# Optimization experiments

Measured on AMD Instinct MI355X. Metric: run time of the kernel, lower is better.

The kernel has to match this reference:

```python
import jax, jax.numpy as jnp
import numpy as np

ACT_BITS = 8
Q_B = 2 ** (ACT_BITS - 1)          # 128
EPS = 1e-6                          # module epsilon
GN_EPS = 1e-5                       # torch GroupNorm default eps
SCALE = 0.01                        # fixed ternary weight scale (buffer)
STRIDE = 1
PADDING = 1


def setup_inputs() -> dict:
    key = jax.random.key(0)
    k1, k2 = jax.random.split(key)
    x = jax.random.normal(k1, (16, 256, 64, 64), dtype=jnp.float32)
    weight = jax.random.normal(k2, (256, 256, 3, 3), dtype=jnp.float32)
    bias = jnp.zeros((256,), dtype=jnp.float32)
    ln_weight = jnp.ones((256,), dtype=jnp.float32)
    ln_bias = jnp.zeros((256,), dtype=jnp.float32)
    return {"x": x, "weight": weight, "bias": bias,
            "ln_weight": ln_weight, "ln_bias": ln_bias}


def _group_norm_1group(x, gamma, beta):
    # GroupNorm(1, C): normalize over (C, H, W) per sample, per-channel affine.
    mean = jnp.mean(x, axis=(1, 2, 3), keepdims=True)
    var = jnp.var(x, axis=(1, 2, 3), keepdims=True)
    xn = (x - mean) * jax.lax.rsqrt(var + GN_EPS)
    return xn * gamma[None, :, None, None] + beta[None, :, None, None]


def reference(x, weight, bias, ln_weight, ln_bias):
    # 1) GroupNorm
    x_ln = _group_norm_1group(x, ln_weight, ln_bias)

    # 2) BitNet absmax activation quantization (global absmax)
    gamma = jnp.maximum(jnp.max(jnp.abs(x_ln)), EPS)
    x_scaled = x_ln * (Q_B / gamma)
    x_clipped = jnp.clip(x_scaled, -Q_B + EPS, Q_B - EPS)
    x_quant = jnp.round(x_clipped)

    # 3) Ternary weight quantization with fixed scale: {-SCALE, 0, +SCALE}
    delta = 0.7 * jnp.mean(jnp.abs(weight))  # TTQ threshold
    w_q = jnp.where(weight > delta, SCALE,
                    jnp.where(weight < -delta, -SCALE, 0.0)).astype(weight.dtype)

    # 4) Conv2d (NCHW, OIHW)
    y = jax.lax.conv_general_dilated(
        x_quant, w_q,
        window_strides=(STRIDE, STRIDE),
        padding=[(PADDING, PADDING), (PADDING, PADDING)],
        dimension_numbers=("NCHW", "OIHW", "NCHW"),
        feature_group_count=1,
    )

    # 5) Dequant + bias
    y = y * (gamma / Q_B) + bias[None, :, None, None]
    return y
```

## Files before the change

### kernel.cpp

```cpp
#include <hip/hip_runtime.h>
#include <hip/hip_bf16.h>

#define CHW   1048576
#define XQ_BYTES 17842176u
#define WQ_OFF   17842176u
#define GNP_OFF  18432000u
#define CMM_OFF  18448384u
#define MR_OFF   18481152u
#define SC_OFF   18481280u
#define WP_OFF   18481296u
#define DL_OFF   18481584u
#define EVC_OFF  18481588u
#define EVL_OFF  18481592u

typedef __attribute__((ext_vector_type(4)))  int i32x4;
typedef __attribute__((ext_vector_type(16))) int i32x16;

__device__ __forceinline__ void gload16(const void* g, void* l) {
    __builtin_amdgcn_global_load_lds(
        (const __attribute__((address_space(1))) unsigned int*)(unsigned long long)(g),
        (__attribute__((address_space(3))) unsigned int*)(unsigned int)(unsigned long long)(l),
        16, 0, 0);
}

__global__ void k_pass1(const float* __restrict__ x, double2* __restrict__ part,
                        float2* __restrict__ cmm) {
    int bid = blockIdx.x;
    int n = bid >> 6, c4 = bid & 63;
    int t = threadIdx.x, ch = t >> 6, lane = t & 63;
    int c = c4 * 4 + ch;
    const float4* p = (const float4*)(x + (size_t)n * CHW + (size_t)c * 4096);
    double s = 0.0, ss = 0.0;
    float mn = 1e30f, mx = -1e30f;
#pragma unroll
    for (int k = 0; k < 16; ++k) {
        float4 v = p[k * 64 + lane];
        mn = fminf(mn, fminf(fminf(v.x, v.y), fminf(v.z, v.w)));
        mx = fmaxf(mx, fmaxf(fmaxf(v.x, v.y), fmaxf(v.z, v.w)));
        double dx = v.x, dy = v.y, dz = v.z, dw = v.w;
        s  += dx + dy + dz + dw;
        ss += dx * dx + dy * dy + dz * dz + dw * dw;
    }
    for (int o = 32; o; o >>= 1) {
        s += __shfl_down(s, o); ss += __shfl_down(ss, o);
        mn = fminf(mn, __shfl_down(mn, o)); mx = fmaxf(mx, __shfl_down(mx, o));
    }
    __shared__ double sh0[4], sh1[4];
    if (lane == 0) {
        cmm[n * 256 + c] = make_float2(mn, mx);
        sh0[ch] = s; sh1[ch] = ss;
    }
    __syncthreads();
    if (t == 0)
        part[bid] = make_double2(sh0[0] + sh0[1] + sh0[2] + sh0[3],
                                 sh1[0] + sh1[1] + sh1[2] + sh1[3]);
}

__global__ void k_wsum(const float* __restrict__ w, double* __restrict__ wp) {
    int blk = blockIdx.x, t = threadIdx.x;
    const float4* p = (const float4*)(w + (size_t)blk * 16384);
    double s = 0.0;
#pragma unroll
    for (int j = 0; j < 16; ++j) {
        float4 v = p[j * 256 + t];
        s += fabs((double)v.x) + fabs((double)v.y) + fabs((double)v.z) + fabs((double)v.w);
    }
    for (int o = 32; o; o >>= 1) s += __shfl_down(s, o);
    __shared__ double sh[4];
    if ((t & 63) == 0) sh[t >> 6] = s;
    __syncthreads();
    if (t == 0) wp[blk] = sh[0] + sh[1] + sh[2] + sh[3];
}

__global__ void k_scalars(const double2* __restrict__ part, const float2* __restrict__ cmm,
                          const float* __restrict__ lnw, const float* __restrict__ lnb,
                          const double* __restrict__ wp,
                          float2* __restrict__ mr, float* __restrict__ sc,
                          float* __restrict__ dl, int* __restrict__ evcnt) {
    __shared__ float shm[16], shr[16];
    int t = threadIdx.x;
    {
        int n = t >> 4, i = t & 15;
        double s = 0.0, ss = 0.0;
#pragma unroll
        for (int k = 0; k < 4; ++k) {
            double2 v = part[n * 64 + i * 4 + k];
            s += v.x; ss += v.y;
        }
        for (int o = 8; o; o >>= 1) { s += __shfl_down(s, o); ss += __shfl_down(ss, o); }
        if (i == 0) {
            double mean = s * (1.0 / 1048576.0);
            double var  = ss * (1.0 / 1048576.0) - mean * mean;
            shm[n] = (float)mean; shr[n] = (float)(1.0 / sqrt(var + 1e-5));
        }
    }
    __syncthreads();
    if (t < 16) mr[t] = make_float2(shm[t], shr[t]);
    if (t == 0) evcnt[0] = 0;
    float m = 0.0f;
#pragma unroll
    for (int k = 0; k < 16; ++k) {
        int idx = t + k * 256;
        int n = idx >> 8, c = idx & 255;
        float2 v = cmm[idx];
        float scale = lnw[c] * shr[n];
        float shift = lnb[c] - shm[n] * scale;
        m = fmaxf(m, fmaxf(fabsf(v.x * scale + shift), fabsf(v.y * scale + shift)));
    }
    for (int o = 32; o; o >>= 1) m = fmaxf(m, __shfl_down(m, o));
    __shared__ float shg[4];
    if ((t & 63) == 0) shg[t >> 6] = m;
    __syncthreads();
    if (t == 0) {
        float gamma = fmaxf(fmaxf(fmaxf(shg[0], shg[1]), fmaxf(shg[2], shg[3])), 1e-6f);
        sc[0] = gamma;
        sc[1] = 128.0f / gamma;
        sc[2] = (gamma / 128.0f) * 0.01f;
    }
    if (t < 64) {
        double s = (t < 36) ? wp[t] : 0.0;
        for (int o = 32; o; o >>= 1) s += __shfl_down(s, o);
        if (t == 0) dl[0] = (float)(0.7 * (s / 589824.0));
    }
}

__global__ void k_wquant(const float* __restrict__ w, const float* __restrict__ dl,
                         signed char* __restrict__ wq) {
    __shared__ float sw[2304];
    int co = blockIdx.x, t = threadIdx.x;
    const float* wr = w + (size_t)co * 2304;
#pragma unroll
    for (int j = 0; j < 9; ++j) sw[j * 256 + t] = wr[j * 256 + t];
    __syncthreads();
    float d = dl[0];
#pragma unroll
    for (int tap = 0; tap < 9; ++tap) {
        float v = sw[t * 9 + tap];
        int s = (v > d) ? 1 : ((v < -d) ? -1 : 0);
        wq[tap * 65536 + co * 256 + t] = (signed char)s;
    }
}

__global__ void k_halo(unsigned char* __restrict__ xq) {
    int idx = blockIdx.x * 8 + (threadIdx.x >> 5);
    int n = idx / 260, p = idx - n * 260;
    int hh, ww;
    if (p < 66)       { hh = 0;        ww = p; }
    else if (p < 132) { hh = 65;       ww = p - 66; }
    else if (p < 196) { hh = p - 131;  ww = 0; }
    else              { hh = p - 195;  ww = 65; }
    *(uint2*)(xq + ((size_t)(n * 66 + hh) * 66 + ww) * 256 + (threadIdx.x & 31) * 8) =
        make_uint2(0, 0);
}

__global__ void k_quantx(const float* __restrict__ x, const float2* __restrict__ mr,
                         const float* __restrict__ sc, const float* __restrict__ lnw,
                         const float* __restrict__ lnb, unsigned char* __restrict__ xq,
                         int* __restrict__ evcnt, int* __restrict__ evlist) {
    int bid = blockIdx.x;
    int n = bid >> 6, hg = (bid >> 2) & 15, cg = bid & 3;
    int t = threadIdx.x;
    int w = t & 63, h = hg * 4 + (t >> 6);
    float2 m = mr[n];
    float s128 = sc[1];
    uint u[16];
    const float* xp = x + (((size_t)n * 256 + cg * 64) * 64 + h) * 64 + w;
#pragma unroll
    for (int ci = 0; ci < 64; ++ci) {
        int c = cg * 64 + ci;
        float g = lnw[c] * m.y;
        float be = lnb[c];
        float v = xp[(size_t)ci * 4096];
        float xs = ((v - m.x) * g + be) * s128;
        xs = fminf(fmaxf(xs, -(128.0f - 1e-6f)), 128.0f - 1e-6f);
        int q = (int)rintf(xs);
        if (q == 128) {
            int idx = atomicAdd(evcnt, 1);
            if (idx < 1024) evlist[idx] = (n << 20) | (h << 14) | (w << 8) | c;
            q = 127;
        }
        uint b = (uint)(q & 255);
        if ((ci & 3) == 0) u[ci >> 2] = b; else u[ci >> 2] |= b << ((ci & 3) * 8);
    }
    unsigned char* op = xq + ((size_t)(n * 66 + h + 1) * 66 + (w + 1)) * 256 + cg * 64;
    uint4* o4 = (uint4*)op;
#pragma unroll
    for (int s2 = 0; s2 < 4; ++s2)
        o4[s2] = make_uint4(u[s2 * 4], u[s2 * 4 + 1], u[s2 * 4 + 2], u[s2 * 4 + 3]);
}

__global__ void k_fix(const signed char* __restrict__ wq, const int* __restrict__ evcnt,
                      const int* __restrict__ evlist, const float* __restrict__ sc,
                      float* __restrict__ out) {
    int cnt = *evcnt; if (cnt > 1024) cnt = 1024;
    float qs = sc[2];
    int co = threadIdx.x;
    for (int e = blockIdx.x; e < cnt; e += gridDim.x) {
        int pk = evlist[e];
        int n = pk >> 20, h = (pk >> 14) & 63, w = (pk >> 8) & 63, ci = pk & 255;
#pragma unroll
        for (int ty = 0; ty < 3; ++ty)
#pragma unroll
            for (int tx = 0; tx < 3; ++tx) {
                int i = h + 1 - ty, j = w + 1 - tx;
                if (i < 0 || i > 63 || j < 0 || j > 63) continue;
                int sgn = wq[(ty * 3 + tx) * 65536 + co * 256 + ci];
                if (sgn)
                    atomicAdd(out + (((size_t)n * 256 + co) * 64 + i) * 64 + j,
                              qs * (float)sgn);
            }
    }
}

#define ABUFB 32768
#define LD16(off) (*(const i32x4*)&lds8[(off)])
#define MFMA_I8(A, B, C) __builtin_amdgcn_mfma_i32_32x32x32_i8(A, B, C, 0, 0, 0)

#define STAGE_A(AS) { \
    const int _so = (AS) * ABUFB + wv * 1024; \
    gload16(aSrc + stA,         lds8 + _so); \
    gload16(aSrc + stA + 33792, lds8 + _so + 8192); \
    if (aKc < 3) { aKc++; stA += 64; } \
    else { aKc = 0; if (aTx < 2) { aTx++; stA += 64; } else { aTx = 0; stA += 16192; } } }

#define STAGE_B(BS) { \
    const int _so = (BS) * ABUFB + 16384 + wv * 1024; \
    gload16(bSrc + stB,         lds8 + _so); \
    gload16(bSrc + stB + 32768, lds8 + _so + 8192); \
    if (bKc < 3) { bKc++; stB += 64; } else { bKc = 0; stB += 65344; } }

#define PHASE(RB, SB, DO, W) { \
    const int _ab = (RB) * ABUFB; \
    const int _bb = (RB) * ABUFB + 16384; \
    i32x4 a00 = LD16(_ab + rdA),        a01 = LD16((_ab + rdA) ^ 32); \
    i32x4 a10 = LD16(_ab + rdA + 2048), a11 = LD16((_ab + rdA + 2048) ^ 32); \
    i32x4 a20 = LD16(_ab + rdA + 4096), a21 = LD16((_ab + rdA + 4096) ^ 32); \
    i32x4 a30 = LD16(_ab + rdA + 6144), a31 = LD16((_ab + rdA + 6144) ^ 32); \
    i32x4 b00 = LD16(_bb + rdB),        b01 = LD16((_bb + rdB) ^ 32); \
    i32x4 b10 = LD16(_bb + rdB + 2048), b11 = LD16((_bb + rdB + 2048) ^ 32); \
    if (DO) { STAGE_A(SB) STAGE_B(SB) } \
    __builtin_amdgcn_sched_barrier(0); \
    __builtin_amdgcn_s_barrier(); \
    asm volatile("s_waitcnt lgkmcnt(0)" ::: "memory"); \
    __builtin_amdgcn_sched_barrier(0); \
    __builtin_amdgcn_s_setprio(1); \
    acc[0][0] = MFMA_I8(a00, b00, acc[0][0]); acc[0][1] = MFMA_I8(a00, b10, acc[0][1]); \
    acc[1][0] = MFMA_I8(a10, b00, acc[1][0]); acc[1][1] = MFMA_I8(a10, b10, acc[1][1]); \
    acc[2][0] = MFMA_I8(a20, b00, acc[2][0]); acc[2][1] = MFMA_I8(a20, b10, acc[2][1]); \
    acc[3][0] = MFMA_I8(a30, b00, acc[3][0]); acc[3][1] = MFMA_I8(a30, b10, acc[3][1]); \
    acc[0][0] = MFMA_I8(a01, b01, acc[0][0]); acc[0][1] = MFMA_I8(a01, b11, acc[0][1]); \
    acc[1][0] = MFMA_I8(a11, b01, acc[1][0]); acc[1][1] = MFMA_I8(a11, b11, acc[1][1]); \
    acc[2][0] = MFMA_I8(a21, b01, acc[2][0]); acc[2][1] = MFMA_I8(a21, b11, acc[2][1]); \
    acc[3][0] = MFMA_I8(a31, b01, acc[3][0]); acc[3][1] = MFMA_I8(a31, b11, acc[3][1]); \
    __builtin_amdgcn_s_setprio(0); \
    if ((W) == 8)      { asm volatile("s_waitcnt vmcnt(8)" ::: "memory"); } \
    else if ((W) == 4) { asm volatile("s_waitcnt vmcnt(4)" ::: "memory"); } \
    else if ((W) == 0) { asm volatile("s_waitcnt vmcnt(0)" ::: "memory"); } \
    if ((W) >= 0) { __builtin_amdgcn_s_barrier(); __builtin_amdgcn_sched_barrier(0); } \
}

__global__ __launch_bounds__(512, 2) void k_conv(const unsigned char* __restrict__ xq,
                                                 const signed char* __restrict__ wq,
                                                 const float* __restrict__ sc,
                                                 const float* __restrict__ bias,
                                                 float* __restrict__ out) {
    __shared__ __align__(128) unsigned char lds8[163840];
    int t = threadIdx.x, wv = t >> 6, l = t & 63;
    int wm = wv >> 2, wn = wv & 3;
    int l31 = l & 31, l5 = l >> 5;

    int bid = ((int)blockIdx.x & 7) * 32 + ((int)blockIdx.x >> 3);
    int n = bid >> 4, h2 = (bid & 15) << 2;

    int s_src = (l & 7) ^ (l >> 3);
    int sb2   = (s_src >> 2) & 1;
    int skc   = s_src & 3;
    int RA    = wv * 16 + ((l >> 3) << 1) + sb2;
    int hsub  = RA >> 6, wA = RA & 63;
    const unsigned char* aSrc = xq +
        ((size_t)(n * 66 + h2 + hsub) * 66 + wA) * 256 + skc * 16;
    int coB = ((wv * 8 + (l >> 3)) << 1) + sb2;
    const unsigned char* bSrc = (const unsigned char*)wq + (size_t)coB * 256 + skc * 16;

    int q3    = (l31 >> 1) & 7;
    int s0    = ((l31 & 1) << 2) | l5;
    int phys0 = s0 ^ q3;
    int rdA = (wm * 64 + (l31 >> 1)) * 128 + phys0 * 16;
    int rdB = (wn * 32 + (l31 >> 1)) * 128 + phys0 * 16;

    i32x16 acc[4][2] = {};

    int stA = 0, aKc = 0, aTx = 0;
    int stB = 0, bKc = 0;
    STAGE_A(0) STAGE_B(0)
    STAGE_A(1) STAGE_B(1)
    STAGE_A(2) STAGE_B(2)
    asm volatile("s_waitcnt vmcnt(8)" ::: "memory");
    __builtin_amdgcn_s_barrier();
    __builtin_amdgcn_sched_barrier(0);

#pragma unroll 1
    for (int it = 0; it < 6; ++it) {
        PHASE(0, 3, 1, 8)
        PHASE(1, 4, 1, 8)
        PHASE(2, 0, 1, 8)
        PHASE(3, 1, 1, 8)
        PHASE(4, 2, 1, 8)
    }
    PHASE(0, 3, 1, 8)
    PHASE(1, 4, 1, 8)
    PHASE(2, 0, 1, 8)
    PHASE(3, 0, 0, 4)
    PHASE(4, 0, 0, 0)
    PHASE(0, 0, 0, -1)

    float qs = sc[2];
    float bv0 = bias[wn * 64 + l31];
    float bv1 = bias[wn * 64 + 32 + l31];
    __builtin_amdgcn_s_barrier();
    float4* lf = (float4*)lds8;
#pragma unroll
    for (int rh = 0; rh < 2; ++rh) {
#pragma unroll
        for (int mh = 0; mh < 2; ++mh) {
            int m = rh * 2 + mh;
#pragma unroll
            for (int nf = 0; nf < 2; ++nf) {
                int co = wn * 64 + nf * 32 + l31;
                float bv = nf ? bv1 : bv0;
                int rowb = (wm * 256 + co) * 16;
#pragma unroll
                for (int rg = 0; rg < 4; ++rg) {
                    int slot = mh * 8 + rg * 2 + l5;
                    float4 v;
                    v.x = (float)acc[m][nf][rg * 4 + 0] * qs + bv;
                    v.y = (float)acc[m][nf][rg * 4 + 1] * qs + bv;
                    v.z = (float)acc[m][nf][rg * 4 + 2] * qs + bv;
                    v.w = (float)acc[m][nf][rg * 4 + 3] * qs + bv;
                    lf[rowb + (slot ^ (co & 7))] = v;
                }
            }
        }
        __syncthreads();
#pragma unroll
        for (int i = 0; i < 16; ++i) {
            int idx = t + i * 512;
            int lw = idx & 15, co = (idx >> 4) & 255, hs = idx >> 12;
            float4 v = lf[(hs * 256 + co) * 16 + (lw ^ (co & 7))];
            int h = h2 + hs * 2 + rh;
            *(float4*)(out + ((size_t)(n * 256 + co) * 64 + h) * 64 + lw * 4) = v;
        }
        if (rh == 0) __syncthreads();
    }
}

extern "C" void kernel_launch(void* const* d_in, const int* in_sizes, int n_in,
                              void* d_out, int out_size, void* d_ws, size_t ws_size,
                              hipStream_t stream) {
    (void)in_sizes; (void)n_in; (void)out_size; (void)ws_size;
    const float* x    = (const float*)d_in[0];
    const float* wgt  = (const float*)d_in[1];
    const float* bias = (const float*)d_in[2];
    const float* lnw  = (const float*)d_in[3];
    const float* lnb  = (const float*)d_in[4];
    float* out = (float*)d_out;
    char* ws = (char*)d_ws;

    unsigned char* xq  = (unsigned char*)ws;
    signed char*   wq  = (signed char*)(ws + WQ_OFF);
    double2* gnp = (double2*)(ws + GNP_OFF);
    float2*  cmm = (float2*)(ws + CMM_OFF);
    float2*  mr  = (float2*)(ws + MR_OFF);
    float*   sc  = (float*)(ws + SC_OFF);
    double*  wp  = (double*)(ws + WP_OFF);
    float*   dl  = (float*)(ws + DL_OFF);
    int*     evc = (int*)(ws + EVC_OFF);
    int*     evl = (int*)(ws + EVL_OFF);

    k_pass1  <<<1024, 256, 0, stream>>>(x, gnp, cmm);
    k_wsum   <<<36,   256, 0, stream>>>(wgt, wp);
    k_scalars<<<1,    256, 0, stream>>>(gnp, cmm, lnw, lnb, wp, mr, sc, dl, evc);
    k_wquant <<<256,  256, 0, stream>>>(wgt, dl, wq);
    k_halo   <<<520,  256, 0, stream>>>(xq);
    k_quantx <<<1024, 256, 0, stream>>>(x, mr, sc, lnw, lnb, xq, evc, evl);
    k_conv   <<<256,  512, 0, stream>>>(xq, wq, sc, bias, out);
    k_fix    <<<64,   256, 0, stream>>>(wq, evc, evl, sc, out);
}
```

Measured before the change: 102.2 us.

## Double-buffer LDS fragments in registers to overlap reads with MFMAs

Restructures the conv main loop so LDS fragment reads for the next buffer are issued before the MFMAs of the current buffer, using two register sets (E/O) in a ping-pong pattern. The barrier and vmcnt wait move to the start of each phase, and the per-phase lgkmcnt(0) wait before the MFMAs is removed. The goal is to hide LDS read latency behind matrix math. In exchange it needs about 24 more VGPRs, which may pressure occupancy under launch_bounds(512,2). The vmcnt wait changes from 8 to 4, which may add stalls on global loads.

```diff
diff --git a/kernel.cpp b/kernel.cpp
--- a/kernel.cpp
+++ b/kernel.cpp
@@ -229,34 +229,34 @@
     gload16(bSrc + stB + 32768, lds8 + _so + 8192); \
     if (bKc < 3) { bKc++; stB += 64; } else { bKc = 0; stB += 65344; } }
 
-#define PHASE(RB, SB, DO, W) { \
-    const int _ab = (RB) * ABUFB; \
-    const int _bb = (RB) * ABUFB + 16384; \
-    i32x4 a00 = LD16(_ab + rdA),        a01 = LD16((_ab + rdA) ^ 32); \
-    i32x4 a10 = LD16(_ab + rdA + 2048), a11 = LD16((_ab + rdA + 2048) ^ 32); \
-    i32x4 a20 = LD16(_ab + rdA + 4096), a21 = LD16((_ab + rdA + 4096) ^ 32); \
-    i32x4 a30 = LD16(_ab + rdA + 6144), a31 = LD16((_ab + rdA + 6144) ^ 32); \
-    i32x4 b00 = LD16(_bb + rdB),        b01 = LD16((_bb + rdB) ^ 32); \
-    i32x4 b10 = LD16(_bb + rdB + 2048), b11 = LD16((_bb + rdB + 2048) ^ 32); \
-    if (DO) { STAGE_A(SB) STAGE_B(SB) } \
-    __builtin_amdgcn_sched_barrier(0); \
-    __builtin_amdgcn_s_barrier(); \
-    asm volatile("s_waitcnt lgkmcnt(0)" ::: "memory"); \
-    __builtin_amdgcn_sched_barrier(0); \
-    __builtin_amdgcn_s_setprio(1); \
-    acc[0][0] = MFMA_I8(a00, b00, acc[0][0]); acc[0][1] = MFMA_I8(a00, b10, acc[0][1]); \
-    acc[1][0] = MFMA_I8(a10, b00, acc[1][0]); acc[1][1] = MFMA_I8(a10, b10, acc[1][1]); \
-    acc[2][0] = MFMA_I8(a20, b00, acc[2][0]); acc[2][1] = MFMA_I8(a20, b10, acc[2][1]); \
-    acc[3][0] = MFMA_I8(a30, b00, acc[3][0]); acc[3][1] = MFMA_I8(a30, b10, acc[3][1]); \
-    acc[0][0] = MFMA_I8(a01, b01, acc[0][0]); acc[0][1] = MFMA_I8(a01, b11, acc[0][1]); \
-    acc[1][0] = MFMA_I8(a11, b01, acc[1][0]); acc[1][1] = MFMA_I8(a11, b11, acc[1][1]); \
-    acc[2][0] = MFMA_I8(a21, b01, acc[2][0]); acc[2][1] = MFMA_I8(a21, b11, acc[2][1]); \
-    acc[3][0] = MFMA_I8(a31, b01, acc[3][0]); acc[3][1] = MFMA_I8(a31, b11, acc[3][1]); \
-    __builtin_amdgcn_s_setprio(0); \
-    if ((W) == 8)      { asm volatile("s_waitcnt vmcnt(8)" ::: "memory"); } \
-    else if ((W) == 4) { asm volatile("s_waitcnt vmcnt(4)" ::: "memory"); } \
+#define LOADF(S, RB) { \
+    const int _ab = (RB) * ABUFB; const int _bb = _ab + 16384; \
+    S##a00 = LD16(_ab + rdA);        S##a01 = LD16((_ab + rdA) ^ 32); \
+    S##a10 = LD16(_ab + rdA + 2048); S##a11 = LD16((_ab + rdA + 2048) ^ 32); \
+    S##a20 = LD16(_ab + rdA + 4096); S##a21 = LD16((_ab + rdA + 4096) ^ 32); \
+    S##a30 = LD16(_ab + rdA + 6144); S##a31 = LD16((_ab + rdA + 6144) ^ 32); \
+    S##b00 = LD16(_bb + rdB);        S##b01 = LD16((_bb + rdB) ^ 32); \
+    S##b10 = LD16(_bb + rdB + 2048); S##b11 = LD16((_bb + rdB + 2048) ^ 32); }
+
+#define MFMAS(S) \
+    acc[0][0] = MFMA_I8(S##a00, S##b00, acc[0][0]); acc[0][1] = MFMA_I8(S##a00, S##b10, acc[0][1]); \
+    acc[1][0] = MFMA_I8(S##a10, S##b00, acc[1][0]); acc[1][1] = MFMA_I8(S##a10, S##b10, acc[1][1]); \
+    acc[2][0] = MFMA_I8(S##a20, S##b00, acc[2][0]); acc[2][1] = MFMA_I8(S##a20, S##b10, acc[2][1]); \
+    acc[3][0] = MFMA_I8(S##a30, S##b00, acc[3][0]); acc[3][1] = MFMA_I8(S##a30, S##b10, acc[3][1]); \
+    acc[0][0] = MFMA_I8(S##a01, S##b01, acc[0][0]); acc[0][1] = MFMA_I8(S##a01, S##b11, acc[0][1]); \
+    acc[1][0] = MFMA_I8(S##a11, S##b01, acc[1][0]); acc[1][1] = MFMA_I8(S##a11, S##b11, acc[1][1]); \
+    acc[2][0] = MFMA_I8(S##a21, S##b01, acc[2][0]); acc[2][1] = MFMA_I8(S##a21, S##b11, acc[2][1]); \
+    acc[3][0] = MFMA_I8(S##a31, S##b01, acc[3][0]); acc[3][1] = MFMA_I8(S##a31, S##b11, acc[3][1]);
+
+#define PHASEP(RBN, SB, DO, W, L, C) { \
+    if ((W) == 4)      { asm volatile("s_waitcnt vmcnt(4)" ::: "memory"); } \
     else if ((W) == 0) { asm volatile("s_waitcnt vmcnt(0)" ::: "memory"); } \
     if ((W) >= 0) { __builtin_amdgcn_s_barrier(); __builtin_amdgcn_sched_barrier(0); } \
+    if ((RBN) >= 0) LOADF(L, RBN) \
+    if (DO) { STAGE_A(SB) STAGE_B(SB) } \
+    __builtin_amdgcn_s_setprio(1); \
+    MFMAS(C) \
+    __builtin_amdgcn_s_setprio(0); \
 }
 
 __global__ __launch_bounds__(512, 2) void k_conv(const unsigned char* __restrict__ xq,
@@ -289,6 +289,8 @@
     int rdB = (wn * 32 + (l31 >> 1)) * 128 + phys0 * 16;
 
     i32x16 acc[4][2] = {};
+    i32x4 Ea00, Ea01, Ea10, Ea11, Ea20, Ea21, Ea30, Ea31, Eb00, Eb01, Eb10, Eb11;
+    i32x4 Oa00, Oa01, Oa10, Oa11, Oa20, Oa21, Oa30, Oa31, Ob00, Ob01, Ob10, Ob11;
 
     int stA = 0, aKc = 0, aTx = 0;
     int stB = 0, bKc = 0;
@@ -298,21 +300,27 @@
     asm volatile("s_waitcnt vmcnt(8)" ::: "memory");
     __builtin_amdgcn_s_barrier();
     __builtin_amdgcn_sched_barrier(0);
+    LOADF(E, 0)
 
 #pragma unroll 1
-    for (int it = 0; it < 6; ++it) {
-        PHASE(0, 3, 1, 8)
-        PHASE(1, 4, 1, 8)
-        PHASE(2, 0, 1, 8)
-        PHASE(3, 1, 1, 8)
-        PHASE(4, 2, 1, 8)
-    }
-    PHASE(0, 3, 1, 8)
-    PHASE(1, 4, 1, 8)
-    PHASE(2, 0, 1, 8)
-    PHASE(3, 0, 0, 4)
-    PHASE(4, 0, 0, 0)
-    PHASE(0, 0, 0, -1)
+    for (int it = 0; it < 3; ++it) {
+        PHASEP(1, 3, 1, 4, O, E)
+        PHASEP(2, 4, 1, 4, E, O)
+        PHASEP(3, 0, 1, 4, O, E)
+        PHASEP(4, 1, 1, 4, E, O)
+        PHASEP(0, 2, 1, 4, O, E)
+        PHASEP(1, 3, 1, 4, E, O)
+        PHASEP(2, 4, 1, 4, O, E)
+        PHASEP(3, 0, 1, 4, E, O)
+        PHASEP(4, 1, 1, 4, O, E)
+        PHASEP(0, 2, 1, 4, E, O)
+    }
+    PHASEP(1, 3, 1, 4, O, E)
+    PHASEP(2, 4, 1, 4, E, O)
+    PHASEP(3, 0, 1, 4, O, E)
+    PHASEP(4, 0, 0, 4, E, O)
+    PHASEP(0, 0, 0, 0, O, E)
+    PHASEP(-1, 0, 0, -1, E, O)
 
     float qs = sc[2];
     float bv0 = bias[wn * 64 + l31];
```

Result: slower. 146.6 us (median of 2 runs) (+43.5%).

## Software-pipeline LDS fragment loads across phases with register double buffering

Applied to the files above, without the earlier changes.

The conv main loop now splits each phase's MFMA work into two half-K chunks. The first-half fragments of the next LDS buffer are preloaded into alternating register sets (U/V) while the current MFMAs run. The per-phase pre-MFMA barrier with full lgkmcnt drain is replaced by a partial lgkmcnt wait, the vmcnt waits are tightened from 8 to 4 outstanding loads, and the loop is unrolled by 10 phases to alternate register sets. It also drops the occupancy hint of 2 blocks per CU from launch_bounds, which raises register pressure and risks spills or scheduling changes in exchange for better LDS/MFMA overlap.

```diff
diff --git a/kernel.cpp b/kernel.cpp
--- a/kernel.cpp
+++ b/kernel.cpp
@@ -229,41 +229,56 @@
     gload16(bSrc + stB + 32768, lds8 + _so + 8192); \
     if (bKc < 3) { bKc++; stB += 64; } else { bKc = 0; stB += 65344; } }
 
-#define PHASE(RB, SB, DO, W) { \
+#define PHASE(RB, RBN, SB, DO, W, CUR, NXT) { \
     const int _ab = (RB) * ABUFB; \
-    const int _bb = (RB) * ABUFB + 16384; \
-    i32x4 a00 = LD16(_ab + rdA),        a01 = LD16((_ab + rdA) ^ 32); \
-    i32x4 a10 = LD16(_ab + rdA + 2048), a11 = LD16((_ab + rdA + 2048) ^ 32); \
-    i32x4 a20 = LD16(_ab + rdA + 4096), a21 = LD16((_ab + rdA + 4096) ^ 32); \
-    i32x4 a30 = LD16(_ab + rdA + 6144), a31 = LD16((_ab + rdA + 6144) ^ 32); \
-    i32x4 b00 = LD16(_bb + rdB),        b01 = LD16((_bb + rdB) ^ 32); \
-    i32x4 b10 = LD16(_bb + rdB + 2048), b11 = LD16((_bb + rdB + 2048) ^ 32); \
+    const int _bb = _ab + 16384; \
+    i32x4 sb0 = LD16((_bb + rdB) ^ 32);        i32x4 sb1 = LD16((_bb + rdB + 2048) ^ 32); \
+    i32x4 sa0 = LD16((_ab + rdA) ^ 32);        i32x4 sa1 = LD16((_ab + rdA + 2048) ^ 32); \
+    i32x4 sa2 = LD16((_ab + rdA + 4096) ^ 32); i32x4 sa3 = LD16((_ab + rdA + 6144) ^ 32); \
     if (DO) { STAGE_A(SB) STAGE_B(SB) } \
-    __builtin_amdgcn_sched_barrier(0); \
-    __builtin_amdgcn_s_barrier(); \
-    asm volatile("s_waitcnt lgkmcnt(0)" ::: "memory"); \
+    asm volatile("s_waitcnt lgkmcnt(6)" ::: "memory"); \
     __builtin_amdgcn_sched_barrier(0); \
     __builtin_amdgcn_s_setprio(1); \
-    acc[0][0] = MFMA_I8(a00, b00, acc[0][0]); acc[0][1] = MFMA_I8(a00, b10, acc[0][1]); \
-    acc[1][0] = MFMA_I8(a10, b00, acc[1][0]); acc[1][1] = MFMA_I8(a10, b10, acc[1][1]); \
-    acc[2][0] = MFMA_I8(a20, b00, acc[2][0]); acc[2][1] = MFMA_I8(a20, b10, acc[2][1]); \
-    acc[3][0] = MFMA_I8(a30, b00, acc[3][0]); acc[3][1] = MFMA_I8(a30, b10, acc[3][1]); \
-    acc[0][0] = MFMA_I8(a01, b01, acc[0][0]); acc[0][1] = MFMA_I8(a01, b11, acc[0][1]); \
-    acc[1][0] = MFMA_I8(a11, b01, acc[1][0]); acc[1][1] = MFMA_I8(a11, b11, acc[1][1]); \
-    acc[2][0] = MFMA_I8(a21, b01, acc[2][0]); acc[2][1] = MFMA_I8(a21, b11, acc[2][1]); \
-    acc[3][0] = MFMA_I8(a31, b01, acc[3][0]); acc[3][1] = MFMA_I8(a31, b11, acc[3][1]); \
+    acc[0][0] = MFMA_I8(CUR##a0, CUR##b0, acc[0][0]); \
+    acc[1][0] = MFMA_I8(CUR##a1, CUR##b0, acc[1][0]); \
+    acc[2][0] = MFMA_I8(CUR##a2, CUR##b0, acc[2][0]); \
+    acc[3][0] = MFMA_I8(CUR##a3, CUR##b0, acc[3][0]); \
+    acc[0][1] = MFMA_I8(CUR##a0, CUR##b1, acc[0][1]); \
+    acc[1][1] = MFMA_I8(CUR##a1, CUR##b1, acc[1][1]); \
+    acc[2][1] = MFMA_I8(CUR##a2, CUR##b1, acc[2][1]); \
+    acc[3][1] = MFMA_I8(CUR##a3, CUR##b1, acc[3][1]); \
     __builtin_amdgcn_s_setprio(0); \
-    if ((W) == 8)      { asm volatile("s_waitcnt vmcnt(8)" ::: "memory"); } \
-    else if ((W) == 4) { asm volatile("s_waitcnt vmcnt(4)" ::: "memory"); } \
+    __builtin_amdgcn_sched_barrier(0); \
+    if ((RBN) >= 0) { \
+        const int _abn = (RBN) * ABUFB; const int _bbn = _abn + 16384; \
+        NXT##b0 = LD16(_bbn + rdB);        NXT##b1 = LD16(_bbn + rdB + 2048); \
+        NXT##a0 = LD16(_abn + rdA);        NXT##a1 = LD16(_abn + rdA + 2048); \
+        NXT##a2 = LD16(_abn + rdA + 4096); NXT##a3 = LD16(_abn + rdA + 6144); \
+        asm volatile("s_waitcnt lgkmcnt(6)" ::: "memory"); \
+    } else { \
+        asm volatile("s_waitcnt lgkmcnt(0)" ::: "memory"); \
+    } \
+    __builtin_amdgcn_sched_barrier(0); \
+    __builtin_amdgcn_s_setprio(1); \
+    acc[0][0] = MFMA_I8(sa0, sb0, acc[0][0]); \
+    acc[1][0] = MFMA_I8(sa1, sb0, acc[1][0]); \
+    acc[2][0] = MFMA_I8(sa2, sb0, acc[2][0]); \
+    acc[3][0] = MFMA_I8(sa3, sb0, acc[3][0]); \
+    acc[0][1] = MFMA_I8(sa0, sb1, acc[0][1]); \
+    acc[1][1] = MFMA_I8(sa1, sb1, acc[1][1]); \
+    acc[2][1] = MFMA_I8(sa2, sb1, acc[2][1]); \
+    acc[3][1] = MFMA_I8(sa3, sb1, acc[3][1]); \
+    __builtin_amdgcn_s_setprio(0); \
+    if ((W) == 4)      { asm volatile("s_waitcnt vmcnt(4)" ::: "memory"); } \
     else if ((W) == 0) { asm volatile("s_waitcnt vmcnt(0)" ::: "memory"); } \
     if ((W) >= 0) { __builtin_amdgcn_s_barrier(); __builtin_amdgcn_sched_barrier(0); } \
 }
 
-__global__ __launch_bounds__(512, 2) void k_conv(const unsigned char* __restrict__ xq,
-                                                 const signed char* __restrict__ wq,
-                                                 const float* __restrict__ sc,
-                                                 const float* __restrict__ bias,
-                                                 float* __restrict__ out) {
+__global__ __launch_bounds__(512) void k_conv(const unsigned char* __restrict__ xq,
+                                              const signed char* __restrict__ wq,
+                                              const float* __restrict__ sc,
+                                              const float* __restrict__ bias,
+                                              float* __restrict__ out) {
     __shared__ __align__(128) unsigned char lds8[163840];
     int t = threadIdx.x, wv = t >> 6, l = t & 63;
     int wm = wv >> 2, wn = wv & 3;
@@ -289,30 +304,40 @@
     int rdB = (wn * 32 + (l31 >> 1)) * 128 + phys0 * 16;
 
     i32x16 acc[4][2] = {};
+    i32x4 Ua0, Ua1, Ua2, Ua3, Ub0, Ub1;
+    i32x4 Va0, Va1, Va2, Va3, Vb0, Vb1;
 
     int stA = 0, aKc = 0, aTx = 0;
     int stB = 0, bKc = 0;
     STAGE_A(0) STAGE_B(0)
     STAGE_A(1) STAGE_B(1)
     STAGE_A(2) STAGE_B(2)
-    asm volatile("s_waitcnt vmcnt(8)" ::: "memory");
+    asm volatile("s_waitcnt vmcnt(4)" ::: "memory");
     __builtin_amdgcn_s_barrier();
     __builtin_amdgcn_sched_barrier(0);
+    Ub0 = LD16(16384 + rdB); Ub1 = LD16(16384 + rdB + 2048);
+    Ua0 = LD16(rdA);         Ua1 = LD16(rdA + 2048);
+    Ua2 = LD16(rdA + 4096);  Ua3 = LD16(rdA + 6144);
 
 #pragma unroll 1
-    for (int it = 0; it < 6; ++it) {
-        PHASE(0, 3, 1, 8)
-        PHASE(1, 4, 1, 8)
-        PHASE(2, 0, 1, 8)
-        PHASE(3, 1, 1, 8)
-        PHASE(4, 2, 1, 8)
-    }
-    PHASE(0, 3, 1, 8)
-    PHASE(1, 4, 1, 8)
-    PHASE(2, 0, 1, 8)
-    PHASE(3, 0, 0, 4)
-    PHASE(4, 0, 0, 0)
-    PHASE(0, 0, 0, -1)
+    for (int it = 0; it < 3; ++it) {
+        PHASE(0, 1, 3, 1, 4, U, V)
+        PHASE(1, 2, 4, 1, 4, V, U)
+        PHASE(2, 3, 0, 1, 4, U, V)
+        PHASE(3, 4, 1, 1, 4, V, U)
+        PHASE(4, 0, 2, 1, 4, U, V)
+        PHASE(0, 1, 3, 1, 4, V, U)
+        PHASE(1, 2, 4, 1, 4, U, V)
+        PHASE(2, 3, 0, 1, 4, V, U)
+        PHASE(3, 4, 1, 1, 4, U, V)
+        PHASE(4, 0, 2, 1, 4, V, U)
+    }
+    PHASE(0, 1, 3, 1, 4, U, V)
+    PHASE(1, 2, 4, 1, 4, V, U)
+    PHASE(2, 3, 0, 1, 4, U, V)
+    PHASE(3, 4, 0, 0, 0, V, U)
+    PHASE(4, 0, 0, 0, 0, U, V)
+    PHASE(0, -1, 0, 0, -1, V, U)
 
     float qs = sc[2];
     float bv0 = bias[wn * 64 + l31];
```

Measured after the change: 100.4 us. No clear change (-1.8%).

## Split conv tile over output channels with 256-thread blocks and triple buffering

Applied to the files above, without the earlier changes.

The implicit-GEMM conv block tile changes from 256 pixels × 256 output channels with 512 threads to 256 pixels × 128 channels with 256 threads. The grid doubles to 512 blocks, the LDS pipeline drops from five stages to three (72KB), and the LDS fragment loads are interleaved with MFMAs per row-slice instead of all being loaded before one barrier. The aim is better occupancy and overlap of LDS reads with MFMA work. The cost is that each activation tile is now loaded twice, once per channel half, and arithmetic intensity per block is lower.

```diff
diff --git a/kernel.cpp b/kernel.cpp
--- a/kernel.cpp
+++ b/kernel.cpp
@@ -212,81 +212,76 @@
     }
 }
 
-#define ABUFB 32768
+#define BUFB 24576
 #define LD16(off) (*(const i32x4*)&lds8[(off)])
 #define MFMA_I8(A, B, C) __builtin_amdgcn_mfma_i32_32x32x32_i8(A, B, C, 0, 0, 0)
 
 #define STAGE_A(AS) { \
-    const int _so = (AS) * ABUFB + wv * 1024; \
-    gload16(aSrc + stA,         lds8 + _so); \
-    gload16(aSrc + stA + 33792, lds8 + _so + 8192); \
+    const int _so = (AS) * BUFB + wv * 1024; \
+    gload16(aSrc + stA,          lds8 + _so); \
+    gload16(aSrc + stA + 16896,  lds8 + _so + 4096); \
+    gload16(aSrc + stA + 33792,  lds8 + _so + 8192); \
+    gload16(aSrc + stA + 50688,  lds8 + _so + 12288); \
     if (aKc < 3) { aKc++; stA += 64; } \
     else { aKc = 0; if (aTx < 2) { aTx++; stA += 64; } else { aTx = 0; stA += 16192; } } }
 
 #define STAGE_B(BS) { \
-    const int _so = (BS) * ABUFB + 16384 + wv * 1024; \
-    gload16(bSrc + stB,         lds8 + _so); \
-    gload16(bSrc + stB + 32768, lds8 + _so + 8192); \
+    const int _so = (BS) * BUFB + 16384 + wv * 1024; \
+    gload16(bSrc + stB,          lds8 + _so); \
+    gload16(bSrc + stB + 16384,  lds8 + _so + 4096); \
     if (bKc < 3) { bKc++; stB += 64; } else { bKc = 0; stB += 65344; } }
 
-#define PHASE(RB, SB, DO, W) { \
-    const int _ab = (RB) * ABUFB; \
-    const int _bb = (RB) * ABUFB + 16384; \
-    i32x4 a00 = LD16(_ab + rdA),        a01 = LD16((_ab + rdA) ^ 32); \
-    i32x4 a10 = LD16(_ab + rdA + 2048), a11 = LD16((_ab + rdA + 2048) ^ 32); \
-    i32x4 a20 = LD16(_ab + rdA + 4096), a21 = LD16((_ab + rdA + 4096) ^ 32); \
-    i32x4 a30 = LD16(_ab + rdA + 6144), a31 = LD16((_ab + rdA + 6144) ^ 32); \
-    i32x4 b00 = LD16(_bb + rdB),        b01 = LD16((_bb + rdB) ^ 32); \
-    i32x4 b10 = LD16(_bb + rdB + 2048), b11 = LD16((_bb + rdB + 2048) ^ 32); \
+#define ITER(RB, SB, DO, W) { \
+    const int _ab = (RB) * BUFB; \
     if (DO) { STAGE_A(SB) STAGE_B(SB) } \
-    __builtin_amdgcn_sched_barrier(0); \
-    __builtin_amdgcn_s_barrier(); \
-    asm volatile("s_waitcnt lgkmcnt(0)" ::: "memory"); \
-    __builtin_amdgcn_sched_barrier(0); \
-    __builtin_amdgcn_s_setprio(1); \
-    acc[0][0] = MFMA_I8(a00, b00, acc[0][0]); acc[0][1] = MFMA_I8(a00, b10, acc[0][1]); \
-    acc[1][0] = MFMA_I8(a10, b00, acc[1][0]); acc[1][1] = MFMA_I8(a10, b10, acc[1][1]); \
-    acc[2][0] = MFMA_I8(a20, b00, acc[2][0]); acc[2][1] = MFMA_I8(a20, b10, acc[2][1]); \
-    acc[3][0] = MFMA_I8(a30, b00, acc[3][0]); acc[3][1] = MFMA_I8(a30, b10, acc[3][1]); \
-    acc[0][0] = MFMA_I8(a01, b01, acc[0][0]); acc[0][1] = MFMA_I8(a01, b11, acc[0][1]); \
-    acc[1][0] = MFMA_I8(a11, b01, acc[1][0]); acc[1][1] = MFMA_I8(a11, b11, acc[1][1]); \
-    acc[2][0] = MFMA_I8(a21, b01, acc[2][0]); acc[2][1] = MFMA_I8(a21, b11, acc[2][1]); \
-    acc[3][0] = MFMA_I8(a31, b01, acc[3][0]); acc[3][1] = MFMA_I8(a31, b11, acc[3][1]); \
-    __builtin_amdgcn_s_setprio(0); \
-    if ((W) == 8)      { asm volatile("s_waitcnt vmcnt(8)" ::: "memory"); } \
-    else if ((W) == 4) { asm volatile("s_waitcnt vmcnt(4)" ::: "memory"); } \
+    i32x4 b00 = LD16(_ab + rdB);          i32x4 b01 = LD16((_ab + rdB) ^ 32); \
+    i32x4 b10 = LD16(_ab + rdB + 2048);   i32x4 b11 = LD16((_ab + rdB + 2048) ^ 32); \
+    _Pragma("unroll") \
+    for (int _m = 0; _m < 4; ++_m) { \
+        const int _ra = _ab + rdA + _m * 2048; \
+        i32x4 a0 = LD16(_ra); \
+        i32x4 a1 = LD16(_ra ^ 32); \
+        __builtin_amdgcn_s_setprio(1); \
+        acc[_m][0] = MFMA_I8(a0, b00, acc[_m][0]); \
+        acc[_m][1] = MFMA_I8(a0, b10, acc[_m][1]); \
+        acc[_m][0] = MFMA_I8(a1, b01, acc[_m][0]); \
+        acc[_m][1] = MFMA_I8(a1, b11, acc[_m][1]); \
+        __builtin_amdgcn_s_setprio(0); \
+    } \
+    if ((W) == 6)      { asm volatile("s_waitcnt vmcnt(6)" ::: "memory"); } \
     else if ((W) == 0) { asm volatile("s_waitcnt vmcnt(0)" ::: "memory"); } \
     if ((W) >= 0) { __builtin_amdgcn_s_barrier(); __builtin_amdgcn_sched_barrier(0); } \
 }
 
-__global__ __launch_bounds__(512, 2) void k_conv(const unsigned char* __restrict__ xq,
-                                                 const signed char* __restrict__ wq,
-                                                 const float* __restrict__ sc,
-                                                 const float* __restrict__ bias,
-                                                 float* __restrict__ out) {
-    __shared__ __align__(128) unsigned char lds8[163840];
+__global__ __launch_bounds__(256) void k_conv(const unsigned char* __restrict__ xq,
+                                              const signed char* __restrict__ wq,
+                                              const float* __restrict__ sc,
+                                              const float* __restrict__ bias,
+                                              float* __restrict__ out) {
+    __shared__ __align__(128) unsigned char lds8[73728];
     int t = threadIdx.x, wv = t >> 6, l = t & 63;
-    int wm = wv >> 2, wn = wv & 3;
+    int wm = wv >> 1, wn = wv & 1;
     int l31 = l & 31, l5 = l >> 5;
 
-    int bid = ((int)blockIdx.x & 7) * 32 + ((int)blockIdx.x >> 3);
-    int n = bid >> 4, h2 = (bid & 15) << 2;
+    int bid = ((int)blockIdx.x & 7) * 64 + ((int)blockIdx.x >> 3);
+    int n = bid >> 5, rem = bid & 31;
+    int h2 = ((rem >> 1) & 15) << 2, c2 = rem & 1;
 
     int s_src = (l & 7) ^ (l >> 3);
     int sb2   = (s_src >> 2) & 1;
     int skc   = s_src & 3;
     int RA    = wv * 16 + ((l >> 3) << 1) + sb2;
-    int hsub  = RA >> 6, wA = RA & 63;
     const unsigned char* aSrc = xq +
-        ((size_t)(n * 66 + h2 + hsub) * 66 + wA) * 256 + skc * 16;
-    int coB = ((wv * 8 + (l >> 3)) << 1) + sb2;
-    const unsigned char* bSrc = (const unsigned char*)wq + (size_t)coB * 256 + skc * 16;
+        ((size_t)(n * 66 + h2) * 66 + RA) * 256 + skc * 16;
+    int coB = wv * 16 + ((l >> 3) << 1) + sb2;
+    const unsigned char* bSrc = (const unsigned char*)wq +
+        (size_t)(c2 * 128 + coB) * 256 + skc * 16;
 
     int q3    = (l31 >> 1) & 7;
     int s0    = ((l31 & 1) << 2) | l5;
     int phys0 = s0 ^ q3;
     int rdA = (wm * 64 + (l31 >> 1)) * 128 + phys0 * 16;
-    int rdB = (wn * 32 + (l31 >> 1)) * 128 + phys0 * 16;
+    int rdB = 16384 + (wn * 32 + (l31 >> 1)) * 128 + phys0 * 16;
 
     i32x16 acc[4][2] = {};
 
@@ -294,29 +289,23 @@
     int stB = 0, bKc = 0;
     STAGE_A(0) STAGE_B(0)
     STAGE_A(1) STAGE_B(1)
-    STAGE_A(2) STAGE_B(2)
-    asm volatile("s_waitcnt vmcnt(8)" ::: "memory");
+    asm volatile("s_waitcnt vmcnt(6)" ::: "memory");
     __builtin_amdgcn_s_barrier();
     __builtin_amdgcn_sched_barrier(0);
 
 #pragma unroll 1
-    for (int it = 0; it < 6; ++it) {
-        PHASE(0, 3, 1, 8)
-        PHASE(1, 4, 1, 8)
-        PHASE(2, 0, 1, 8)
-        PHASE(3, 1, 1, 8)
-        PHASE(4, 2, 1, 8)
-    }
-    PHASE(0, 3, 1, 8)
-    PHASE(1, 4, 1, 8)
-    PHASE(2, 0, 1, 8)
-    PHASE(3, 0, 0, 4)
-    PHASE(4, 0, 0, 0)
-    PHASE(0, 0, 0, -1)
+    for (int it = 0; it < 11; ++it) {
+        ITER(0, 2, 1, 6)
+        ITER(1, 0, 1, 6)
+        ITER(2, 1, 1, 6)
+    }
+    ITER(0, 2, 1, 6)
+    ITER(1, 0, 0, 0)
+    ITER(2, 0, 0, -1)
 
     float qs = sc[2];
-    float bv0 = bias[wn * 64 + l31];
-    float bv1 = bias[wn * 64 + 32 + l31];
+    float bv0 = bias[c2 * 128 + wn * 64 + l31];
+    float bv1 = bias[c2 * 128 + wn * 64 + 32 + l31];
     __builtin_amdgcn_s_barrier();
     float4* lf = (float4*)lds8;
 #pragma unroll
@@ -326,9 +315,9 @@
             int m = rh * 2 + mh;
 #pragma unroll
             for (int nf = 0; nf < 2; ++nf) {
-                int co = wn * 64 + nf * 32 + l31;
+                int co128 = wn * 64 + nf * 32 + l31;
                 float bv = nf ? bv1 : bv0;
-                int rowb = (wm * 256 + co) * 16;
+                int rowb = (wm * 128 + co128) * 16;
 #pragma unroll
                 for (int rg = 0; rg < 4; ++rg) {
                     int slot = mh * 8 + rg * 2 + l5;
@@ -337,17 +326,18 @@
                     v.y = (float)acc[m][nf][rg * 4 + 1] * qs + bv;
                     v.z = (float)acc[m][nf][rg * 4 + 2] * qs + bv;
                     v.w = (float)acc[m][nf][rg * 4 + 3] * qs + bv;
-                    lf[rowb + (slot ^ (co & 7))] = v;
+                    lf[rowb + (slot ^ (co128 & 7))] = v;
                 }
             }
         }
         __syncthreads();
 #pragma unroll
         for (int i = 0; i < 16; ++i) {
-            int idx = t + i * 512;
-            int lw = idx & 15, co = (idx >> 4) & 255, hs = idx >> 12;
-            float4 v = lf[(hs * 256 + co) * 16 + (lw ^ (co & 7))];
+            int idx = t + i * 256;
+            int lw = idx & 15, co128 = (idx >> 4) & 127, hs = (idx >> 11) & 1;
+            float4 v = lf[(hs * 128 + co128) * 16 + (lw ^ (co128 & 7))];
             int h = h2 + hs * 2 + rh;
+            int co = c2 * 128 + co128;
             *(float4*)(out + ((size_t)(n * 256 + co) * 64 + h) * 64 + lw * 4) = v;
         }
         if (rh == 0) __syncthreads();
@@ -383,6 +373,6 @@
     k_wquant <<<256,  256, 0, stream>>>(wgt, dl, wq);
     k_halo   <<<520,  256, 0, stream>>>(xq);
     k_quantx <<<1024, 256, 0, stream>>>(x, mr, sc, lnw, lnb, xq, evc, evl);
-    k_conv   <<<256,  512, 0, stream>>>(xq, wq, sc, bias, out);
+    k_conv   <<<512,  256, 0, stream>>>(xq, wq, sc, bias, out);
     k_fix    <<<64,   256, 0, stream>>>(wq, evc, evl, sc, out);
 }
```

After: 109.3 us. +7.0%, slower.
